# Kernel optimization log

Measured on AMD Instinct MI355X. Metric: run time of the kernel, lower is better.

## Reference

```python
import jax, jax.numpy as jnp
import numpy as np

LECUN_A = 1.7159
LECUN_B = 0.666


def lecun_tanh(x):
    return LECUN_A * jnp.tanh(LECUN_B * x)


def setup_inputs() -> dict:
    key = jax.random.key(0)
    ks = jax.random.split(key, 12)
    B, T, I, H, U = 128, 1024, 256, 512, 1024
    s_in = 1.0 / np.sqrt(I + H)
    s_u = 1.0 / np.sqrt(U)
    return {
        "input": jax.random.normal(ks[0], (B, T, I), jnp.float32),
        "hx": jax.random.normal(ks[1], (B, T, H), jnp.float32),
        "ts": jax.random.uniform(ks[2], (B, T), jnp.float32),
        "W0": jax.random.normal(ks[3], (I + H, U), jnp.float32) * s_in,
        "b0": jnp.zeros((U,), jnp.float32),
        "W1": jax.random.normal(ks[4], (U, U), jnp.float32) * s_u,
        "b1": jnp.zeros((U,), jnp.float32),
        "W_ff1": jax.random.normal(ks[5], (U, H), jnp.float32) * s_u,
        "b_ff1": jnp.zeros((H,), jnp.float32),
        "W_ff2": jax.random.normal(ks[6], (U, H), jnp.float32) * s_u,
        "b_ff2": jnp.zeros((H,), jnp.float32),
        "W_ta": jax.random.normal(ks[7], (U, H), jnp.float32) * s_u,
        "b_ta": jnp.zeros((H,), jnp.float32),
        "W_tb": jax.random.normal(ks[8], (U, H), jnp.float32) * s_u,
        "b_tb": jnp.zeros((H,), jnp.float32),
    }


def reference(input, hx, ts, W0, b0, W1, b1, W_ff1, b_ff1, W_ff2, b_ff2,
              W_ta, b_ta, W_tb, b_tb):
    # x: [B, T, I+H]
    x = jnp.concatenate([input, hx], axis=2)
    # backbone: Linear -> LeCun -> Linear -> LeCun
    x = lecun_tanh(jnp.einsum("btc,cu->btu", x, W0) + b0)
    x = lecun_tanh(jnp.einsum("btu,uv->btv", x, W1) + b1)
    # four parallel heads sharing x: [B, T, H] each
    ff1 = jnp.tanh(jnp.einsum("btu,uh->bth", x, W_ff1) + b_ff1)
    ff2 = jnp.tanh(jnp.einsum("btu,uh->bth", x, W_ff2) + b_ff2)
    t_a = jnp.einsum("btu,uh->bth", x, W_ta) + b_ta
    t_b = jnp.einsum("btu,uh->bth", x, W_tb) + b_tb
    # time-gated interpolation
    t_interp = jax.nn.sigmoid(t_a * ts[:, :, None] + t_b)
    new_hidden = ff1 * (1.0 - t_interp) + t_interp * ff2
    return new_hidden
```

## Files before the change

kernel.cpp:

```cpp
#include <hip/hip_runtime.h>
#include <hip/hip_bf16.h>


typedef unsigned short u16;
typedef __bf16 bf16x8_t __attribute__((ext_vector_type(8)));
typedef float f32x4_t __attribute__((ext_vector_type(4)));
typedef u16 u16x8_t __attribute__((ext_vector_type(8)));

#define M_TOTAL 131072

__device__ __forceinline__ u16 f2bf(float f) {
  union { float f; unsigned u; } v; v.f = f;
  unsigned r = v.u + 0x7FFFu + ((v.u >> 16) & 1u);
  return (u16)(r >> 16);
}

__device__ __forceinline__ float fast_tanh(float x) {
  x = fminf(15.f, fmaxf(-15.f, x));
  float e = __expf(2.f * x);
  return (e - 1.f) * __builtin_amdgcn_rcpf(e + 1.f);
}

__device__ __forceinline__ float fast_sigmoid(float x) {
  return __builtin_amdgcn_rcpf(1.f + __expf(-x));
}

__device__ __forceinline__ void gload_lds16(const void* g, void* l) {
  __builtin_amdgcn_global_load_lds(
      (const __attribute__((address_space(1))) unsigned int*)g,
      (__attribute__((address_space(3))) unsigned int*)l,
      16, 0, 0);
}


__global__ void prep_x(const float* __restrict__ inp, const float* __restrict__ hx,
                       u16* __restrict__ X) {
  const int total = M_TOTAL * 96;
  int stride = gridDim.x * blockDim.x;
  for (int v = blockIdx.x * blockDim.x + threadIdx.x; v < total; v += stride) {
    int m = v / 96; int c = v - m * 96;
    const float* src = (c < 32) ? (inp + (size_t)m * 256 + (c << 3))
                                : (hx + (size_t)m * 512 + ((size_t)(c - 32) << 3));
    f32x4_t a = *(const f32x4_t*)src;
    f32x4_t b = *(const f32x4_t*)(src + 4);
    u16x8_t o;
    o[0]=f2bf(a[0]); o[1]=f2bf(a[1]); o[2]=f2bf(a[2]); o[3]=f2bf(a[3]);
    o[4]=f2bf(b[0]); o[5]=f2bf(b[1]); o[6]=f2bf(b[2]); o[7]=f2bf(b[3]);
    *(u16x8_t*)(X + (size_t)m * 768 + (c << 3)) = o;
  }
}

__global__ void prep_w(const float* __restrict__ W0, const float* __restrict__ W1,
                       const float* __restrict__ Wf1, const float* __restrict__ Wf2,
                       const float* __restrict__ Wta, const float* __restrict__ Wtb,
                       const float* __restrict__ bf1, const float* __restrict__ bf2,
                       const float* __restrict__ bta, const float* __restrict__ btb,
                       u16* __restrict__ W0T, u16* __restrict__ W1T,
                       u16* __restrict__ WhT, float* __restrict__ biasi) {
  int id = blockIdx.x * blockDim.x + threadIdx.x;
  u16x8_t o;
  if (id < 98304) {
    int n = id / 96, k0 = (id - n * 96) << 3;
#pragma unroll
    for (int i = 0; i < 8; ++i) o[i] = f2bf(W0[(size_t)(k0 + i) * 1024 + n]);
    *(u16x8_t*)(W0T + (size_t)n * 768 + k0) = o;
  } else if (id < 229376) {
    int id2 = id - 98304; int n = id2 >> 7, k0 = (id2 & 127) << 3;
#pragma unroll
    for (int i = 0; i < 8; ++i) o[i] = f2bf(W1[(size_t)(k0 + i) * 1024 + n]);
    *(u16x8_t*)(W1T + (size_t)n * 1024 + k0) = o;
  } else if (id < 491520) {
    int id3 = id - 229376; int head = id3 >> 16; int id4 = id3 & 65535;
    int n = id4 >> 7, k0 = (id4 & 127) << 3;
    const float* W = (head == 0) ? Wf1 : (head == 1) ? Wf2 : (head == 2) ? Wta : Wtb;
#pragma unroll
    for (int i = 0; i < 8; ++i) o[i] = f2bf(W[(size_t)(k0 + i) * 512 + n]);
    int row = ((n >> 4) << 6) + head * 16 + (n & 15);
    *(u16x8_t*)(WhT + (size_t)row * 1024 + k0) = o;
  } else if (id < 492032) {
    int h = id - 491520;
    int base = ((h >> 4) << 6) + (h & 15);
    biasi[base +  0] = bf1[h];
    biasi[base + 16] = bf2[h];
    biasi[base + 32] = bta[h];
    biasi[base + 48] = btb[h];
  }
}


#define BARX()  do { __builtin_amdgcn_s_barrier(); __builtin_amdgcn_sched_barrier(0); } while(0)
#define LGKM0() do { asm volatile("s_waitcnt lgkmcnt(0)" ::: "memory"); __builtin_amdgcn_sched_barrier(0); } while(0)
#define VMC4()  do { asm volatile("s_waitcnt vmcnt(4)" ::: "memory"); } while(0)

template<int K, int NI, int EPI, int TPB>
__global__ __launch_bounds__(512, 2)
void gemm256(const u16* __restrict__ A, const u16* __restrict__ BT,
             const float* __restrict__ bias, const float* __restrict__ ts,
             void* __restrict__ Cout)
{
  constexpr int NTn = NI / 256;
  constexpr int NITER = K / 128;
  __shared__ __align__(16) char smem[131072];

  const int tid = threadIdx.x;
  const int w = tid >> 6, l = tid & 63;
  const int wm = w >> 2, wn = w & 3;

  const int c0 = w * 2, c1 = w * 2 + 1;
  const int kkS0 = c0 >> 3, kkS1 = c1 >> 3;
  const int rS0 = (c0 & 7) * 16 + (l >> 2);
  const int rS1 = (c1 & 7) * 16 + (l >> 2);
  const int cbS = ((l & 3) << 4) ^ (((l >> 5) & 1) << 5);
  const int cA0 = (c0 & 7) * 1024, cA1 = (c1 & 7) * 1024;
  const int laneK = cbS >> 1;

  const int colRs = ((l >> 4) * 16) ^ (((l >> 3) & 1) << 5);
  const int aRowB = (wm * 128 + (l & 15)) * 64;
  const int bRowB = 65536 + (wn * 64 + (l & 15)) * 64;

  f32x4_t acc[8][4];
  bf16x8_t af[4][2], b01[2][2], b23[2][2];

#define STAGE_A(d, h, SRC, t) do { \
    gload_lds16((SRC) + (size_t)((h)*128 + rS0) * K + (t)*64 + kkS0*32, \
                smem + (d)*32768 + kkS0*16384 + (h)*8192 + cA0); \
    gload_lds16((SRC) + (size_t)((h)*128 + rS1) * K + (t)*64 + kkS1*32, \
                smem + (d)*32768 + kkS1*16384 + (h)*8192 + cA1); } while(0)

#define STAGE_B(d, h, SRC, t) do { \
    gload_lds16((SRC) + (size_t)((h)*128 + rS0) * K + (t)*64 + kkS0*32, \
                smem + 65536 + (d)*32768 + kkS0*16384 + (h)*8192 + cA0); \
    gload_lds16((SRC) + (size_t)((h)*128 + rS1) * K + (t)*64 + kkS1*32, \
                smem + 65536 + (d)*32768 + kkS1*16384 + (h)*8192 + cA1); } while(0)

#define READ_A(d, mb) do { \
    _Pragma("unroll") for (int mm_ = 0; mm_ < 4; ++mm_) { \
      af[mm_][0] = *(const bf16x8_t*)(smem + (d)*32768 +         aRowB + ((mb)+mm_)*1024 + colRs); \
      af[mm_][1] = *(const bf16x8_t*)(smem + (d)*32768 + 16384 + aRowB + ((mb)+mm_)*1024 + colRs); } } while(0)

#define READ_B(d, breg, nb) do { \
    _Pragma("unroll") for (int nn_ = 0; nn_ < 2; ++nn_) { \
      breg[nn_][0] = *(const bf16x8_t*)(smem + (d)*32768 +         bRowB + ((nb)+nn_)*1024 + colRs); \
      breg[nn_][1] = *(const bf16x8_t*)(smem + (d)*32768 + 16384 + bRowB + ((nb)+nn_)*1024 + colRs); } } while(0)

#define MFMAQ(mb, nb, breg) do { \
    __builtin_amdgcn_s_setprio(1); \
    _Pragma("unroll") for (int kk_ = 0; kk_ < 2; ++kk_) \
      _Pragma("unroll") for (int mm_ = 0; mm_ < 4; ++mm_) \
        _Pragma("unroll") for (int nn_ = 0; nn_ < 2; ++nn_) \
          acc[(mb)+mm_][(nb)+nn_] = __builtin_amdgcn_mfma_f32_16x16x32_bf16( \
              af[mm_][kk_], breg[nn_][kk_], acc[(mb)+mm_][(nb)+nn_], 0, 0, 0); \
    __builtin_amdgcn_s_setprio(0); \
  } while(0)

#define ITER(ii, A2, B2, T2, T3) do { \
    READ_A(0, 0); READ_B(0, b01, 0); \
    STAGE_A(1, 0, aCur, 2*(ii)+1); \
    BARX(); LGKM0(); MFMAQ(0, 0, b01); BARX(); \
    READ_B(0, b23, 2); \
    STAGE_A(1, 1, aCur, 2*(ii)+1); \
    BARX(); LGKM0(); MFMAQ(0, 2, b23); BARX(); \
    READ_A(0, 4); \
    STAGE_B(0, 0, B2, T2); \
    BARX(); LGKM0(); MFMAQ(4, 0, b01); BARX(); \
    STAGE_B(0, 1, B2, T2); \
    BARX(); MFMAQ(4, 2, b23); \
    VMC4(); BARX(); \
    READ_A(1, 0); READ_B(1, b01, 0); \
    STAGE_A(0, 0, A2, T2); \
    BARX(); LGKM0(); MFMAQ(0, 0, b01); BARX(); \
    READ_B(1, b23, 2); \
    STAGE_A(0, 1, A2, T2); \
    BARX(); LGKM0(); MFMAQ(0, 2, b23); BARX(); \
    READ_A(1, 4); \
    STAGE_B(1, 0, B2, T3); \
    BARX(); LGKM0(); MFMAQ(4, 0, b01); BARX(); \
    STAGE_B(1, 1, B2, T3); \
    BARX(); MFMAQ(4, 2, b23); \
    VMC4(); BARX(); \
  } while(0)

  const int tile0 = blockIdx.x * TPB;

  {
    const int mt0 = tile0 / NTn, nt0 = tile0 % NTn;
    const u16* a0 = A + (size_t)(mt0 * 256) * K + laneK;
    const u16* b0 = BT + (size_t)(nt0 * 256) * K + laneK;
    STAGE_A(0, 0, a0, 0); STAGE_A(0, 1, a0, 0);
    STAGE_B(0, 0, b0, 0); STAGE_B(0, 1, b0, 0);
    STAGE_B(1, 0, b0, 1); STAGE_B(1, 1, b0, 1);
    VMC4(); BARX();
  }

#pragma unroll 1
  for (int tt = 0; tt < TPB; ++tt) {
    const int tcur = tile0 + tt;
    const int tnxt = (tt + 1 < TPB) ? tcur + 1 : tcur;
    const int tileM = (tcur / NTn) * 256, tileN = (tcur % NTn) * 256;
    const u16* aCur = A + (size_t)tileM * K + laneK;
    const u16* bCur = BT + (size_t)tileN * K + laneK;
    const u16* aNxt = A + (size_t)((tnxt / NTn) * 256) * K + laneK;
    const u16* bNxt = BT + (size_t)((tnxt % NTn) * 256) * K + laneK;

    const int colBase = tileN + wn * 64 + (l & 15);
    float bv[4];
    bv[0] = bias[colBase];      bv[1] = bias[colBase + 16];
    bv[2] = bias[colBase + 32]; bv[3] = bias[colBase + 48];

#pragma unroll
    for (int i = 0; i < 8; ++i)
#pragma unroll
      for (int j = 0; j < 4; ++j) acc[i][j] = f32x4_t{0.f, 0.f, 0.f, 0.f};

#pragma unroll 1
    for (int i = 0; i < NITER - 1; ++i) ITER(i, aCur, bCur, 2 * i + 2, 2 * i + 3);
    ITER(NITER - 1, aNxt, bNxt, 0, 1);

    if constexpr (EPI == 0) {
      u16* C = (u16*)Cout;
      const int rowB = tileM + wm * 128 + ((l >> 4) << 2);
#pragma unroll
      for (int m = 0; m < 8; ++m)
#pragma unroll
        for (int nn = 0; nn < 4; ++nn)
#pragma unroll
          for (int j = 0; j < 4; ++j) {
            float v = acc[m][nn][j] + bv[nn];
            float t = 1.7159f * fast_tanh(0.666f * v);
            C[(size_t)(rowB + m * 16 + j) * NI + colBase + nn * 16] = f2bf(t);
          }
    } else {
      const int hg = ((tileN + wn * 64) >> 6) * 16 + (l & 15);
      float* out = (float*)Cout;
#pragma unroll
      for (int m = 0; m < 8; ++m)
#pragma unroll
        for (int j = 0; j < 4; ++j) {
          const int rl = wm * 128 + m * 16 + ((l >> 4) << 2) + j;
          const float tsv = ts[tileM + rl];
          float ff1 = fast_tanh(acc[m][0][j] + bv[0]);
          float ff2 = fast_tanh(acc[m][1][j] + bv[1]);
          float s = fast_sigmoid((acc[m][2][j] + bv[2]) * tsv + (acc[m][3][j] + bv[3]));
          out[(size_t)(tileM + rl) * 512 + hg] = ff1 + s * (ff2 - ff1);
        }
    }
  }

  asm volatile("s_waitcnt vmcnt(0)" ::: "memory");

#undef STAGE_A
#undef STAGE_B
#undef READ_A
#undef READ_B
#undef MFMAQ
#undef ITER
}


extern "C" void kernel_launch(void* const* d_in, const int* in_sizes, int n_in,
                              void* d_out, int out_size, void* d_ws, size_t ws_size,
                              hipStream_t stream) {
  const float* input = (const float*)d_in[0];
  const float* hx    = (const float*)d_in[1];
  const float* ts    = (const float*)d_in[2];
  const float* W0    = (const float*)d_in[3];
  const float* b0    = (const float*)d_in[4];
  const float* W1    = (const float*)d_in[5];
  const float* b1    = (const float*)d_in[6];
  const float* Wff1  = (const float*)d_in[7];
  const float* bff1  = (const float*)d_in[8];
  const float* Wff2  = (const float*)d_in[9];
  const float* bff2  = (const float*)d_in[10];
  const float* Wta   = (const float*)d_in[11];
  const float* bta   = (const float*)d_in[12];
  const float* Wtb   = (const float*)d_in[13];
  const float* btb   = (const float*)d_in[14];

  const size_t WS_NEEDED = 544743424ull;
  if (ws_size < WS_NEEDED) return;
  char* ws = (char*)d_ws;
  u16* Xcat = (u16*)(ws);
  u16* X2   = (u16*)(ws);
  u16* X1   = (u16*)(ws + 268435456ull);
  u16* W0T  = (u16*)(ws + 536870912ull);
  u16* W1T  = (u16*)(ws + 538443776ull);
  u16* WhT  = (u16*)(ws + 540540928ull);
  float* biasi = (float*)(ws + 544735232ull);

  prep_x<<<2048, 256, 0, stream>>>(input, hx, Xcat);
  prep_w<<<1922, 256, 0, stream>>>(W0, W1, Wff1, Wff2, Wta, Wtb,
                                   bff1, bff2, bta, btb, W0T, W1T, WhT, biasi);

  gemm256<768, 1024, 0, 8><<<256, 512, 0, stream>>>(Xcat, W0T, b0, nullptr, X1);
  gemm256<1024, 1024, 0, 8><<<256, 512, 0, stream>>>(X1, W1T, b1, nullptr, X2);
  gemm256<1024, 2048, 1, 16><<<256, 512, 0, stream>>>(X2, WhT, biasi, ts, d_out);
}
```

Baseline: 1.398 ms.

## Replace persistent multi-tile GEMM with one-tile-per-block 4-stage LDS pipeline

The persistent kernel, which walked 8 or 16 output tiles per block with a hand-interleaved 2-buffer schedule, is replaced by a non-persistent launch of one 256x256 tile per workgroup. A 4-slot circular LDS buffer stages K=32 slices three steps ahead, with vmcnt-based waits and a single barrier per step. Block IDs are remapped so the eight interleaved groups of blocks cover contiguous tile ranges. The aim is deeper prefetch, simpler synchronisation and better load balance. The cost is losing the overlap of one tile's epilogue and prologue with the next tile's loads, and having many more workgroups to schedule.

After: 1.243 ms. -11.1%, faster.

```diff
diff --git a/kernel.cpp b/kernel.cpp
--- a/kernel.cpp
+++ b/kernel.cpp
@@ -90,170 +90,129 @@
 
 #define BARX()  do { __builtin_amdgcn_s_barrier(); __builtin_amdgcn_sched_barrier(0); } while(0)
 #define LGKM0() do { asm volatile("s_waitcnt lgkmcnt(0)" ::: "memory"); __builtin_amdgcn_sched_barrier(0); } while(0)
-#define VMC4()  do { asm volatile("s_waitcnt vmcnt(4)" ::: "memory"); } while(0)
-
-template<int K, int NI, int EPI, int TPB>
+#define WAITVM(n) do { asm volatile("s_waitcnt vmcnt(" #n ")" ::: "memory"); __builtin_amdgcn_sched_barrier(0); } while(0)
+
+template<int K, int NI, int EPI>
 __global__ __launch_bounds__(512, 2)
 void gemm256(const u16* __restrict__ A, const u16* __restrict__ BT,
              const float* __restrict__ bias, const float* __restrict__ ts,
              void* __restrict__ Cout)
 {
   constexpr int NTn = NI / 256;
-  constexpr int NITER = K / 128;
+  constexpr int NT = K / 32;
+  constexpr int NWG = (M_TOTAL / 256) * NTn;
   __shared__ __align__(16) char smem[131072];
+
+  const int bid0 = blockIdx.x;
+  const int bid = (bid0 & 7) * (NWG >> 3) + (bid0 >> 3);
+  const int mt = bid / NTn, nt = bid % NTn;
+  const int tileM = mt * 256, tileN = nt * 256;
 
   const int tid = threadIdx.x;
   const int w = tid >> 6, l = tid & 63;
   const int wm = w >> 2, wn = w & 3;
 
-  const int c0 = w * 2, c1 = w * 2 + 1;
-  const int kkS0 = c0 >> 3, kkS1 = c1 >> 3;
-  const int rS0 = (c0 & 7) * 16 + (l >> 2);
-  const int rS1 = (c1 & 7) * 16 + (l >> 2);
   const int cbS = ((l & 3) << 4) ^ (((l >> 5) & 1) << 5);
-  const int cA0 = (c0 & 7) * 1024, cA1 = (c1 & 7) * 1024;
   const int laneK = cbS >> 1;
-
-  const int colRs = ((l >> 4) * 16) ^ (((l >> 3) & 1) << 5);
-  const int aRowB = (wm * 128 + (l & 15)) * 64;
-  const int bRowB = 65536 + (wn * 64 + (l & 15)) * 64;
+  const int rA = 32 * w + (l >> 2);
+  const u16* aS0 = A + (size_t)(tileM + rA) * K + laneK;
+  const u16* aS1 = aS0 + (size_t)16 * K;
+  const u16* bS0 = BT + (size_t)(tileN + rA) * K + laneK;
+  const u16* bS1 = bS0 + (size_t)16 * K;
+  char* ldsA = smem + (w << 11);
+  char* ldsB = smem + 65536 + (w << 11);
+
+  const int colRs = ((l >> 4) << 4) ^ (((l >> 3) & 1) << 5);
+  const char* aRd = smem + (wm * 128 + (l & 15)) * 64 + colRs;
+  const char* bRd = smem + 65536 + (wn * 64 + (l & 15)) * 64 + colRs;
 
   f32x4_t acc[8][4];
-  bf16x8_t af[4][2], b01[2][2], b23[2][2];
-
-#define STAGE_A(d, h, SRC, t) do { \
-    gload_lds16((SRC) + (size_t)((h)*128 + rS0) * K + (t)*64 + kkS0*32, \
-                smem + (d)*32768 + kkS0*16384 + (h)*8192 + cA0); \
-    gload_lds16((SRC) + (size_t)((h)*128 + rS1) * K + (t)*64 + kkS1*32, \
-                smem + (d)*32768 + kkS1*16384 + (h)*8192 + cA1); } while(0)
-
-#define STAGE_B(d, h, SRC, t) do { \
-    gload_lds16((SRC) + (size_t)((h)*128 + rS0) * K + (t)*64 + kkS0*32, \
-                smem + 65536 + (d)*32768 + kkS0*16384 + (h)*8192 + cA0); \
-    gload_lds16((SRC) + (size_t)((h)*128 + rS1) * K + (t)*64 + kkS1*32, \
-                smem + 65536 + (d)*32768 + kkS1*16384 + (h)*8192 + cA1); } while(0)
-
-#define READ_A(d, mb) do { \
-    _Pragma("unroll") for (int mm_ = 0; mm_ < 4; ++mm_) { \
-      af[mm_][0] = *(const bf16x8_t*)(smem + (d)*32768 +         aRowB + ((mb)+mm_)*1024 + colRs); \
-      af[mm_][1] = *(const bf16x8_t*)(smem + (d)*32768 + 16384 + aRowB + ((mb)+mm_)*1024 + colRs); } } while(0)
-
-#define READ_B(d, breg, nb) do { \
-    _Pragma("unroll") for (int nn_ = 0; nn_ < 2; ++nn_) { \
-      breg[nn_][0] = *(const bf16x8_t*)(smem + (d)*32768 +         bRowB + ((nb)+nn_)*1024 + colRs); \
-      breg[nn_][1] = *(const bf16x8_t*)(smem + (d)*32768 + 16384 + bRowB + ((nb)+nn_)*1024 + colRs); } } while(0)
-
-#define MFMAQ(mb, nb, breg) do { \
+#pragma unroll
+  for (int i = 0; i < 8; ++i)
+#pragma unroll
+    for (int j = 0; j < 4; ++j) acc[i][j] = f32x4_t{0.f, 0.f, 0.f, 0.f};
+
+  bf16x8_t af[8], bfr[4];
+
+#define STAGE_S(t) do { \
+    const int sl_ = ((t) & 3) << 14; \
+    gload_lds16(aS0 + (size_t)(t) * 32, ldsA + sl_); \
+    gload_lds16(aS1 + (size_t)(t) * 32, ldsA + sl_ + 1024); \
+    gload_lds16(bS0 + (size_t)(t) * 32, ldsB + sl_); \
+    gload_lds16(bS1 + (size_t)(t) * 32, ldsB + sl_ + 1024); } while(0)
+
+#define READ_S(s) do { \
+    _Pragma("unroll") for (int n_ = 0; n_ < 4; ++n_) \
+      bfr[n_] = *(const bf16x8_t*)(bRd + (s) * 16384 + n_ * 1024); \
+    _Pragma("unroll") for (int m_ = 0; m_ < 8; ++m_) \
+      af[m_] = *(const bf16x8_t*)(aRd + (s) * 16384 + m_ * 1024); } while(0)
+
+#define MFMA32() do { \
     __builtin_amdgcn_s_setprio(1); \
-    _Pragma("unroll") for (int kk_ = 0; kk_ < 2; ++kk_) \
-      _Pragma("unroll") for (int mm_ = 0; mm_ < 4; ++mm_) \
-        _Pragma("unroll") for (int nn_ = 0; nn_ < 2; ++nn_) \
-          acc[(mb)+mm_][(nb)+nn_] = __builtin_amdgcn_mfma_f32_16x16x32_bf16( \
-              af[mm_][kk_], breg[nn_][kk_], acc[(mb)+mm_][(nb)+nn_], 0, 0, 0); \
-    __builtin_amdgcn_s_setprio(0); \
-  } while(0)
-
-#define ITER(ii, A2, B2, T2, T3) do { \
-    READ_A(0, 0); READ_B(0, b01, 0); \
-    STAGE_A(1, 0, aCur, 2*(ii)+1); \
-    BARX(); LGKM0(); MFMAQ(0, 0, b01); BARX(); \
-    READ_B(0, b23, 2); \
-    STAGE_A(1, 1, aCur, 2*(ii)+1); \
-    BARX(); LGKM0(); MFMAQ(0, 2, b23); BARX(); \
-    READ_A(0, 4); \
-    STAGE_B(0, 0, B2, T2); \
-    BARX(); LGKM0(); MFMAQ(4, 0, b01); BARX(); \
-    STAGE_B(0, 1, B2, T2); \
-    BARX(); MFMAQ(4, 2, b23); \
-    VMC4(); BARX(); \
-    READ_A(1, 0); READ_B(1, b01, 0); \
-    STAGE_A(0, 0, A2, T2); \
-    BARX(); LGKM0(); MFMAQ(0, 0, b01); BARX(); \
-    READ_B(1, b23, 2); \
-    STAGE_A(0, 1, A2, T2); \
-    BARX(); LGKM0(); MFMAQ(0, 2, b23); BARX(); \
-    READ_A(1, 4); \
-    STAGE_B(1, 0, B2, T3); \
-    BARX(); LGKM0(); MFMAQ(4, 0, b01); BARX(); \
-    STAGE_B(1, 1, B2, T3); \
-    BARX(); MFMAQ(4, 2, b23); \
-    VMC4(); BARX(); \
-  } while(0)
-
-  const int tile0 = blockIdx.x * TPB;
-
-  {
-    const int mt0 = tile0 / NTn, nt0 = tile0 % NTn;
-    const u16* a0 = A + (size_t)(mt0 * 256) * K + laneK;
-    const u16* b0 = BT + (size_t)(nt0 * 256) * K + laneK;
-    STAGE_A(0, 0, a0, 0); STAGE_A(0, 1, a0, 0);
-    STAGE_B(0, 0, b0, 0); STAGE_B(0, 1, b0, 0);
-    STAGE_B(1, 0, b0, 1); STAGE_B(1, 1, b0, 1);
-    VMC4(); BARX();
-  }
+    _Pragma("unroll") for (int m_ = 0; m_ < 8; ++m_) \
+      _Pragma("unroll") for (int n_ = 0; n_ < 4; ++n_) \
+        acc[m_][n_] = __builtin_amdgcn_mfma_f32_16x16x32_bf16( \
+            af[m_], bfr[n_], acc[m_][n_], 0, 0, 0); \
+    __builtin_amdgcn_s_setprio(0); } while(0)
+
+#define STEP(s, vmn, DOST, t) do { \
+    WAITVM(vmn); BARX(); \
+    if (DOST) STAGE_S(t); \
+    READ_S(s); \
+    LGKM0(); \
+    MFMA32(); } while(0)
+
+  STAGE_S(0); STAGE_S(1); STAGE_S(2);
 
 #pragma unroll 1
-  for (int tt = 0; tt < TPB; ++tt) {
-    const int tcur = tile0 + tt;
-    const int tnxt = (tt + 1 < TPB) ? tcur + 1 : tcur;
-    const int tileM = (tcur / NTn) * 256, tileN = (tcur % NTn) * 256;
-    const u16* aCur = A + (size_t)tileM * K + laneK;
-    const u16* bCur = BT + (size_t)tileN * K + laneK;
-    const u16* aNxt = A + (size_t)((tnxt / NTn) * 256) * K + laneK;
-    const u16* bNxt = BT + (size_t)((tnxt % NTn) * 256) * K + laneK;
-
-    const int colBase = tileN + wn * 64 + (l & 15);
-    float bv[4];
-    bv[0] = bias[colBase];      bv[1] = bias[colBase + 16];
-    bv[2] = bias[colBase + 32]; bv[3] = bias[colBase + 48];
-
-#pragma unroll
-    for (int i = 0; i < 8; ++i)
-#pragma unroll
-      for (int j = 0; j < 4; ++j) acc[i][j] = f32x4_t{0.f, 0.f, 0.f, 0.f};
-
-#pragma unroll 1
-    for (int i = 0; i < NITER - 1; ++i) ITER(i, aCur, bCur, 2 * i + 2, 2 * i + 3);
-    ITER(NITER - 1, aNxt, bNxt, 0, 1);
-
-    if constexpr (EPI == 0) {
-      u16* C = (u16*)Cout;
-      const int rowB = tileM + wm * 128 + ((l >> 4) << 2);
-#pragma unroll
-      for (int m = 0; m < 8; ++m)
-#pragma unroll
-        for (int nn = 0; nn < 4; ++nn)
-#pragma unroll
-          for (int j = 0; j < 4; ++j) {
-            float v = acc[m][nn][j] + bv[nn];
-            float t = 1.7159f * fast_tanh(0.666f * v);
-            C[(size_t)(rowB + m * 16 + j) * NI + colBase + nn * 16] = f2bf(t);
-          }
-    } else {
-      const int hg = ((tileN + wn * 64) >> 6) * 16 + (l & 15);
-      float* out = (float*)Cout;
-#pragma unroll
-      for (int m = 0; m < 8; ++m)
+  for (int i = 0; i < NT - 4; i += 4) {
+    STEP(0, 8, true, i + 3);
+    STEP(1, 8, true, i + 4);
+    STEP(2, 8, true, i + 5);
+    STEP(3, 8, true, i + 6);
+  }
+  STEP(0, 8, true, NT - 1);
+  STEP(1, 8, false, 0);
+  STEP(2, 4, false, 0);
+  STEP(3, 0, false, 0);
+
+  const int colBase = tileN + wn * 64 + (l & 15);
+  float bv[4];
+  bv[0] = bias[colBase];      bv[1] = bias[colBase + 16];
+  bv[2] = bias[colBase + 32]; bv[3] = bias[colBase + 48];
+
+  if constexpr (EPI == 0) {
+    u16* C = (u16*)Cout;
+    const int rowB = tileM + wm * 128 + ((l >> 4) << 2);
+#pragma unroll
+    for (int m = 0; m < 8; ++m)
+#pragma unroll
+      for (int nn = 0; nn < 4; ++nn)
 #pragma unroll
         for (int j = 0; j < 4; ++j) {
-          const int rl = wm * 128 + m * 16 + ((l >> 4) << 2) + j;
-          const float tsv = ts[tileM + rl];
-          float ff1 = fast_tanh(acc[m][0][j] + bv[0]);
-          float ff2 = fast_tanh(acc[m][1][j] + bv[1]);
-          float s = fast_sigmoid((acc[m][2][j] + bv[2]) * tsv + (acc[m][3][j] + bv[3]));
-          out[(size_t)(tileM + rl) * 512 + hg] = ff1 + s * (ff2 - ff1);
+          float v = acc[m][nn][j] + bv[nn];
+          float t = 1.7159f * fast_tanh(0.666f * v);
+          C[(size_t)(rowB + m * 16 + j) * NI + colBase + nn * 16] = f2bf(t);
         }
-    }
-  }
-
-  asm volatile("s_waitcnt vmcnt(0)" ::: "memory");
-
-#undef STAGE_A
-#undef STAGE_B
-#undef READ_A
-#undef READ_B
-#undef MFMAQ
-#undef ITER
+  } else {
+    const int hg = ((tileN + wn * 64) >> 6) * 16 + (l & 15);
+    float* out = (float*)Cout;
+#pragma unroll
+    for (int m = 0; m < 8; ++m)
+#pragma unroll
+      for (int j = 0; j < 4; ++j) {
+        const int rl = wm * 128 + m * 16 + ((l >> 4) << 2) + j;
+        const float tsv = ts[tileM + rl];
+        float ff1 = fast_tanh(acc[m][0][j] + bv[0]);
+        float ff2 = fast_tanh(acc[m][1][j] + bv[1]);
+        float s = fast_sigmoid((acc[m][2][j] + bv[2]) * tsv + (acc[m][3][j] + bv[3]));
+        out[(size_t)(tileM + rl) * 512 + hg] = ff1 + s * (ff2 - ff1);
+      }
+  }
+#undef STAGE_S
+#undef READ_S
+#undef MFMA32
+#undef STEP
 }
 
 
@@ -291,7 +250,7 @@
   prep_w<<<1922, 256, 0, stream>>>(W0, W1, Wff1, Wff2, Wta, Wtb,
                                    bff1, bff2, bta, btb, W0T, W1T, WhT, biasi);
 
-  gemm256<768, 1024, 0, 8><<<256, 512, 0, stream>>>(Xcat, W0T, b0, nullptr, X1);
-  gemm256<1024, 1024, 0, 8><<<256, 512, 0, stream>>>(X1, W1T, b1, nullptr, X2);
-  gemm256<1024, 2048, 1, 16><<<256, 512, 0, stream>>>(X2, WhT, biasi, ts, d_out);
-}
+  gemm256<768, 1024, 0><<<2048, 512, 0, stream>>>(Xcat, W0T, b0, nullptr, X1);
+  gemm256<1024, 1024, 0><<<2048, 512, 0, stream>>>(X1, W1T, b1, nullptr, X2);
+  gemm256<1024, 2048, 1><<<4096, 512, 0, stream>>>(X2, WhT, biasi, ts, d_out);
+}
```
